# Kernel tuning notes

Hardware: AMD Instinct MI355X
Metric: run time of the kernel (lower is better)

## Reference

```python
import jax, jax.numpy as jnp
import numpy as np

N_NODES = 100000
N_EDGES = 1600000
D_IN = 64
D_OUT = 64
EDGE_DIM = 16


def setup_inputs() -> dict:
    key = jax.random.key(0)
    ks = jax.random.split(key, 6)
    x = jax.random.normal(ks[0], (N_NODES, D_IN), dtype=jnp.float32)
    edge_index = jax.random.randint(ks[1], (2, N_EDGES), 0, N_NODES, dtype=jnp.int64)
    edge_feature = jax.random.normal(ks[2], (N_EDGES, EDGE_DIM), dtype=jnp.float32)
    W_edge = jax.random.normal(ks[3], (EDGE_DIM, 1), dtype=jnp.float32) * (1.0 / np.sqrt(EDGE_DIM))
    b_edge = jnp.zeros((1,), dtype=jnp.float32)
    W_node = jax.random.normal(ks[4], (D_OUT, D_IN), dtype=jnp.float32) * (1.0 / np.sqrt(D_IN))
    b_node = jnp.zeros((D_OUT,), dtype=jnp.float32)
    return {"x": x, "edge_index": edge_index, "edge_feature": edge_feature,
            "W_edge": W_edge, "b_edge": b_edge, "W_node": W_node, "b_node": b_node}


def reference(x, edge_index, edge_feature, W_edge, b_edge, W_node, b_node):
    # per-edge gate: Linear(edge_dim -> 1) + Sigmoid  -> [E]
    gate = jax.nn.sigmoid(edge_feature @ W_edge + b_edge)[:, 0]
    # node projection: Linear(in -> out)  -> [N, D_OUT]
    xp = x @ W_node.T + b_node
    row = edge_index[0]  # destination (SparseTensor row)
    col = edge_index[1]  # source gathered
    num_nodes = x.shape[0]
    # weighted gather of source node features  -> [E, D_OUT]
    msg = gate[:, None] * xp[col]
    summed = jax.ops.segment_sum(msg, row, num_segments=num_nodes)
    cnt = jax.ops.segment_sum(jnp.ones((row.shape[0],), dtype=xp.dtype), row,
                              num_segments=num_nodes)
    # reduce='mean': divide by row nnz count; empty rows stay 0
    out = summed / jnp.maximum(cnt, 1.0)[:, None]
    return out
```

## Files before the change

kernel.cpp:

```cpp
#include <hip/hip_runtime.h>
#include <math.h>

#define NN 100000
#define NE 1600000
#define DD 64
#define ED 16
#define BROWS 96
#define NBIN 1042
#define NBIN_PAD 1056
#define BCAP 1920
#define EPB 8192
#define NBLKA ((NE + EPB - 1) / EPB)


__device__ __forceinline__ unsigned short f2bf(float f) {
    unsigned int b = __float_as_uint(f);
    unsigned int r = (b + 0x7FFFu + ((b >> 16) & 1u)) >> 16;
    return (unsigned short)r;
}

__global__ __launch_bounds__(256) void proj_kernel(
    const float* __restrict__ x, const float* __restrict__ Wn,
    const float* __restrict__ bn, unsigned short* __restrict__ xpb,
    int* __restrict__ cursor) {
    __shared__ float4 xs[64 * 16];
    int tid = threadIdx.x;
    if (blockIdx.x == 0) {
        for (int i = tid; i < NBIN_PAD; i += 256) cursor[i] = i * BCAP;
    }
    int o = tid & 63;
    int wave = tid >> 6;
    float4 Wr[16];
    const float4* Wn4 = reinterpret_cast<const float4*>(Wn);
#pragma unroll
    for (int k = 0; k < 16; ++k) Wr[k] = Wn4[o * 16 + k];
    float bo = bn[o];
    int n0 = blockIdx.x * 64;
    const float4* x4 = reinterpret_cast<const float4*>(x);
    long base = (long)n0 * 16;
    long limit = (long)NN * 16;
#pragma unroll
    for (int i = 0; i < 4; ++i) {
        long idx = base + tid + 256 * i;
        xs[tid + 256 * i] = (idx < limit) ? x4[idx] : make_float4(0.f, 0.f, 0.f, 0.f);
    }
    __syncthreads();
#pragma unroll
    for (int j = 0; j < 16; ++j) {
        int ln = wave * 16 + j;
        int n = n0 + ln;
        if (n >= NN) break;
        float acc = bo;
#pragma unroll
        for (int k = 0; k < 16; ++k) {
            float4 a = xs[ln * 16 + k];
            acc += a.x * Wr[k].x + a.y * Wr[k].y + a.z * Wr[k].z + a.w * Wr[k].w;
        }
        xpb[(long)n * DD + o] = f2bf(acc);
    }
}

__global__ __launch_bounds__(256) void gate_kernel(
    const float* __restrict__ ef, const float* __restrict__ We,
    const float* __restrict__ be, unsigned short* __restrict__ g16) {
    int e = blockIdx.x * 256 + threadIdx.x;
    if (e >= NE) return;
    const float4* ef4 = reinterpret_cast<const float4*>(ef + (size_t)e * ED);
    const float4* We4 = reinterpret_cast<const float4*>(We);
    float4 a0 = ef4[0], a1 = ef4[1], a2 = ef4[2], a3 = ef4[3];
    float4 w0 = We4[0], w1 = We4[1], w2 = We4[2], w3 = We4[3];
    float d = a0.x * w0.x + a0.y * w0.y + a0.z * w0.z + a0.w * w0.w
            + a1.x * w1.x + a1.y * w1.y + a1.z * w1.z + a1.w * w1.w
            + a2.x * w2.x + a2.y * w2.y + a2.z * w2.z + a2.w * w2.w
            + a3.x * w3.x + a3.y * w3.y + a3.z * w3.z + a3.w * w3.w + be[0];
    float g = 1.f / (1.f + expf(-d));
    int q = (int)(g * 65535.f + 0.5f);
    g16[e] = (unsigned short)min(q, 65535);
}

__global__ __launch_bounds__(1024) void binA_kernel(
    const int* __restrict__ ei, const unsigned short* __restrict__ g16,
    int* __restrict__ cursor, int2* __restrict__ binned) {
    __shared__ int cnt[NBIN_PAD];
    __shared__ int basev[NBIN_PAD];
    int tid = threadIdx.x;
    int e0 = blockIdx.x * EPB;
    cnt[tid] = 0;
    if (tid < NBIN_PAD - 1024) cnt[tid + 1024] = 0;
    __syncthreads();
    int e_base = e0 + tid * 8;
    bool ok = e_base < NE;
    int4 ra, rb, ca, cb;
    ushort4 ga, gb;
    int s0=0,s1=0,s2=0,s3=0,s4=0,s5=0,s6=0,s7=0;
    int b0=0,b1=0,b2=0,b3=0,b4=0,b5=0,b6=0,b7=0;
    if (ok) {
        const int4* pr = reinterpret_cast<const int4*>(ei + e_base);
        ra = pr[0]; rb = pr[1];
        const int4* pc = reinterpret_cast<const int4*>(ei + NE + e_base);
        ca = pc[0]; cb = pc[1];
        const ushort4* pg = reinterpret_cast<const ushort4*>(g16 + e_base);
        ga = pg[0]; gb = pg[1];
        b0 = ra.x / BROWS; s0 = atomicAdd(&cnt[b0], 1);
        b1 = ra.y / BROWS; s1 = atomicAdd(&cnt[b1], 1);
        b2 = ra.z / BROWS; s2 = atomicAdd(&cnt[b2], 1);
        b3 = ra.w / BROWS; s3 = atomicAdd(&cnt[b3], 1);
        b4 = rb.x / BROWS; s4 = atomicAdd(&cnt[b4], 1);
        b5 = rb.y / BROWS; s5 = atomicAdd(&cnt[b5], 1);
        b6 = rb.z / BROWS; s6 = atomicAdd(&cnt[b6], 1);
        b7 = rb.w / BROWS; s7 = atomicAdd(&cnt[b7], 1);
    }
    __syncthreads();
    for (int i = tid; i < NBIN_PAD; i += 1024) {
        int c = cnt[i];
        basev[i] = c ? atomicAdd(&cursor[i], c) : 0;
    }
    __syncthreads();
    if (ok) {
        const float gs = 1.f / 65535.f;
#define EMIT(BV, SV, RR, CC, GG) \
        binned[basev[BV] + SV] = make_int2((((RR) - (BV) * BROWS) << 24) | (CC), \
                                           __float_as_int((float)(GG) * gs));
        EMIT(b0, s0, ra.x, ca.x, ga.x) EMIT(b1, s1, ra.y, ca.y, ga.y)
        EMIT(b2, s2, ra.z, ca.z, ga.z) EMIT(b3, s3, ra.w, ca.w, ga.w)
        EMIT(b4, s4, rb.x, cb.x, gb.x) EMIT(b5, s5, rb.y, cb.y, gb.y)
        EMIT(b6, s6, rb.z, cb.z, gb.z) EMIT(b7, s7, rb.w, cb.w, gb.w)
#undef EMIT
    }
}

__global__ __launch_bounds__(512) void binB_kernel(
    const unsigned short* __restrict__ xpb, const int* __restrict__ cursor,
    const int2* __restrict__ binned, float* __restrict__ out) {
    __shared__ int2 sorted[BCAP];
    __shared__ int hist[128];
    __shared__ int offs[128];
    __shared__ int claim[BROWS];
    int tid = threadIdx.x;
    int b = blockIdx.x;
    if (tid < 128) { hist[tid] = 0; offs[tid] = 0; }
    if (tid < BROWS) claim[tid] = 0;
    __syncthreads();
    int bstart = b * BCAP;
    int nb = cursor[b] - bstart;
    for (int t = tid; t < nb; t += 512) {
        int w = binned[bstart + t].x;
        atomicAdd(&hist[(w >> 24) & 0x7F], 1);
    }
    __syncthreads();
    if (tid < 128) offs[tid] = hist[tid];
    __syncthreads();
    for (int d = 1; d < 128; d <<= 1) {
        int add = 0;
        if (tid < 128 && tid >= d) add = offs[tid - d];
        __syncthreads();
        if (tid < 128) offs[tid] += add;
        __syncthreads();
    }
    for (int t = tid; t < nb; t += 512) {
        int2 e = binned[bstart + t];
        int rl = (e.x >> 24) & 0x7F;
        int pos = offs[rl] - hist[rl] + atomicAdd(&claim[rl], 1);
        sorted[pos] = e;
    }
    __syncthreads();
    int lane = tid & 63;
    int wv = tid >> 6;
    int half = lane >> 5;
    int hl = lane & 31;
#pragma unroll 1
    for (int i = 0; i < 12; ++i) {
        int rl = wv + 8 * i;
        int row = b * BROWS + rl;
        if (row >= NN) break;
        int dn = hist[rl];
        int s0 = offs[rl] - dn;
        float ax = 0.f, ay = 0.f;
        for (int j = 0; j < dn; j += 16) {
#pragma unroll
            for (int k = 0; k < 8; ++k) {
                int ei_ = j + 2 * k + half;
                int2 e = sorted[s0 + min(ei_, dn - 1)];
                float g = (ei_ < dn) ? __int_as_float(e.y) : 0.f;
                int col = e.x & 0x1FFFF;
                unsigned int u = *reinterpret_cast<const unsigned int*>(
                    xpb + (size_t)col * DD + 2 * hl);
                ax += g * __uint_as_float(u << 16);
                ay += g * __uint_as_float(u & 0xFFFF0000u);
            }
        }
        ax += __shfl_xor(ax, 32);
        ay += __shfl_xor(ay, 32);
        if (half == 0) {
            float dv = fmaxf((float)dn, 1.f);
            reinterpret_cast<float2*>(out)[(size_t)row * 32 + hl] =
                make_float2(ax / dv, ay / dv);
        }
    }
}

extern "C" void kernel_launch(void* const* d_in, const int* in_sizes, int n_in,
                              void* d_out, int out_size, void* d_ws, size_t ws_size,
                              hipStream_t stream) {
    const float* x  = (const float*)d_in[0];
    const int*   ei = (const int*)d_in[1];
    const float* ef = (const float*)d_in[2];
    const float* We = (const float*)d_in[3];
    const float* be = (const float*)d_in[4];
    const float* Wn = (const float*)d_in[5];
    const float* bn = (const float*)d_in[6];
    float* out = (float*)d_out;

    unsigned short* xpb = (unsigned short*)d_ws;
    int*  cursor = (int*)d_ws + 3200000;
    unsigned short* g16 = (unsigned short*)((int*)d_ws + 3201056);
    int2* binned = (int2*)((int*)d_ws + 4001056);

    proj_kernel<<<(NN + 63) / 64, 256, 0, stream>>>(x, Wn, bn, xpb, cursor);
    gate_kernel<<<(NE + 255) / 256, 256, 0, stream>>>(ef, We, be, g16);
    binA_kernel<<<NBLKA, 1024, 0, stream>>>(ei, g16, cursor, binned);
    binB_kernel<<<NBIN, 512, 0, stream>>>(xpb, cursor, binned, out);
}
```

Baseline: 117.0 us.

## Register-tile node projection GEMM with 8x4 outputs per thread and padded LDS

Rewrites the node projection kernel as a register-tiled GEMM. Each thread now computes 8 nodes by 4 outputs from padded shared-memory tiles of x and W, and a block covers 128 nodes. This replaces the old scheme of one output per thread with 64 weight registers, aiming to raise arithmetic intensity and to write bf16 outputs as ushort4. It raises register and LDS use per block, and the projection is only a small part of the total pipeline.

```diff
diff --git a/kernel.cpp b/kernel.cpp
--- a/kernel.cpp
+++ b/kernel.cpp
@@ -23,40 +23,67 @@
     const float* __restrict__ x, const float* __restrict__ Wn,
     const float* __restrict__ bn, unsigned short* __restrict__ xpb,
     int* __restrict__ cursor) {
-    __shared__ float4 xs[64 * 16];
+    __shared__ float xs[128][66];
+    __shared__ float ws[64][66];
     int tid = threadIdx.x;
     if (blockIdx.x == 0) {
         for (int i = tid; i < NBIN_PAD; i += 256) cursor[i] = i * BCAP;
     }
-    int o = tid & 63;
-    int wave = tid >> 6;
-    float4 Wr[16];
+    int n0 = blockIdx.x * 128;
+    const float4* x4 = reinterpret_cast<const float4*>(x);
     const float4* Wn4 = reinterpret_cast<const float4*>(Wn);
-#pragma unroll
-    for (int k = 0; k < 16; ++k) Wr[k] = Wn4[o * 16 + k];
-    float bo = bn[o];
-    int n0 = blockIdx.x * 64;
-    const float4* x4 = reinterpret_cast<const float4*>(x);
-    long base = (long)n0 * 16;
     long limit = (long)NN * 16;
 #pragma unroll
+    for (int i = 0; i < 8; ++i) {
+        int idx = tid + 256 * i;
+        int row = idx >> 4, kq = idx & 15;
+        long gidx = (long)n0 * 16 + idx;
+        float4 v = (gidx < limit) ? x4[gidx] : make_float4(0.f, 0.f, 0.f, 0.f);
+        xs[row][kq * 4 + 0] = v.x; xs[row][kq * 4 + 1] = v.y;
+        xs[row][kq * 4 + 2] = v.z; xs[row][kq * 4 + 3] = v.w;
+    }
+#pragma unroll
     for (int i = 0; i < 4; ++i) {
-        long idx = base + tid + 256 * i;
-        xs[tid + 256 * i] = (idx < limit) ? x4[idx] : make_float4(0.f, 0.f, 0.f, 0.f);
-    }
-    __syncthreads();
-#pragma unroll
-    for (int j = 0; j < 16; ++j) {
-        int ln = wave * 16 + j;
-        int n = n0 + ln;
-        if (n >= NN) break;
-        float acc = bo;
-#pragma unroll
-        for (int k = 0; k < 16; ++k) {
-            float4 a = xs[ln * 16 + k];
-            acc += a.x * Wr[k].x + a.y * Wr[k].y + a.z * Wr[k].z + a.w * Wr[k].w;
-        }
-        xpb[(long)n * DD + o] = f2bf(acc);
+        int idx = tid + 256 * i;
+        int row = idx >> 4, kq = idx & 15;
+        float4 v = Wn4[idx];
+        ws[row][kq * 4 + 0] = v.x; ws[row][kq * 4 + 1] = v.y;
+        ws[row][kq * 4 + 2] = v.z; ws[row][kq * 4 + 3] = v.w;
+    }
+    int og = tid & 15;
+    int ng = tid >> 4;
+    float acc[8][4];
+    float b0 = bn[og * 4 + 0], b1 = bn[og * 4 + 1];
+    float b2 = bn[og * 4 + 2], b3 = bn[og * 4 + 3];
+#pragma unroll
+    for (int i = 0; i < 8; ++i) {
+        acc[i][0] = b0; acc[i][1] = b1; acc[i][2] = b2; acc[i][3] = b3;
+    }
+    __syncthreads();
+#pragma unroll 4
+    for (int kk = 0; kk < 32; ++kk) {
+        float2 wv0 = *reinterpret_cast<const float2*>(&ws[og * 4 + 0][kk * 2]);
+        float2 wv1 = *reinterpret_cast<const float2*>(&ws[og * 4 + 1][kk * 2]);
+        float2 wv2 = *reinterpret_cast<const float2*>(&ws[og * 4 + 2][kk * 2]);
+        float2 wv3 = *reinterpret_cast<const float2*>(&ws[og * 4 + 3][kk * 2]);
+#pragma unroll
+        for (int i = 0; i < 8; ++i) {
+            float2 xv = *reinterpret_cast<const float2*>(&xs[ng * 8 + i][kk * 2]);
+            acc[i][0] += xv.x * wv0.x + xv.y * wv0.y;
+            acc[i][1] += xv.x * wv1.x + xv.y * wv1.y;
+            acc[i][2] += xv.x * wv2.x + xv.y * wv2.y;
+            acc[i][3] += xv.x * wv3.x + xv.y * wv3.y;
+        }
+    }
+#pragma unroll
+    for (int i = 0; i < 8; ++i) {
+        int n = n0 + ng * 8 + i;
+        if (n < NN) {
+            ushort4 o;
+            o.x = f2bf(acc[i][0]); o.y = f2bf(acc[i][1]);
+            o.z = f2bf(acc[i][2]); o.w = f2bf(acc[i][3]);
+            *reinterpret_cast<ushort4*>(xpb + (size_t)n * DD + og * 4) = o;
+        }
     }
 }
 
@@ -216,7 +243,7 @@
     unsigned short* g16 = (unsigned short*)((int*)d_ws + 3201056);
     int2* binned = (int2*)((int*)d_ws + 4001056);
 
-    proj_kernel<<<(NN + 63) / 64, 256, 0, stream>>>(x, Wn, bn, xpb, cursor);
+    proj_kernel<<<(NN + 127) / 128, 256, 0, stream>>>(x, Wn, bn, xpb, cursor);
     gate_kernel<<<(NE + 255) / 256, 256, 0, stream>>>(ef, We, be, g16);
     binA_kernel<<<NBLKA, 1024, 0, stream>>>(ei, g16, cursor, binned);
     binB_kernel<<<NBIN, 512, 0, stream>>>(xpb, cursor, binned, out);
```

Result: no change. 116.4 us (-0.6%).
